# Optimization experiments

Hardware: AMD Instinct MI355X
Metric: run time of the kernel (lower is better)

The kernel has to match this reference:

```python
import jax, jax.numpy as jnp
import numpy as np

N_NODES = 500_000
N_EDGES = 16_000_000


def setup_inputs() -> dict:
    key = jax.random.key(0)
    ks = jax.random.split(key, 10)
    x = jax.random.normal(ks[0], (N_NODES, 8), dtype=jnp.float32)
    edge_index = jax.random.randint(ks[1], (2, N_EDGES), 0, N_NODES, dtype=jnp.int64)
    W1_l = jax.random.normal(ks[2], (8, 32), dtype=jnp.float32) * 0.1
    W1_r = jax.random.normal(ks[3], (8, 32), dtype=jnp.float32) * 0.1
    b1 = jax.random.normal(ks[4], (32,), dtype=jnp.float32) * 0.1
    W2_l = jax.random.normal(ks[5], (32, 16), dtype=jnp.float32) * 0.1
    W2_r = jax.random.normal(ks[6], (32, 16), dtype=jnp.float32) * 0.1
    b2 = jax.random.normal(ks[7], (16,), dtype=jnp.float32) * 0.1
    W_out = jax.random.normal(ks[8], (16, 1), dtype=jnp.float32) * 0.1
    b_out = jax.random.normal(ks[9], (1,), dtype=jnp.float32) * 0.1
    return {"x": x, "edge_index": edge_index, "W1_l": W1_l, "W1_r": W1_r, "b1": b1,
            "W2_l": W2_l, "W2_r": W2_r, "b2": b2, "W_out": W_out, "b_out": b_out}


def _sage_conv(x, src, dst, deg_inv, W_l, W_r, b):
    # mean-aggregate neighbor features: gather x[src], scatter-add to dst, divide by degree
    agg = jax.ops.segment_sum(x[src], dst, num_segments=N_NODES)  # [N, d_in]
    mean_nb = agg * deg_inv[:, None]
    return mean_nb @ W_l + x @ W_r + b


def reference(x, edge_index, W1_l, W1_r, b1, W2_l, W2_r, b2, W_out, b_out):
    src, dst = edge_index[0], edge_index[1]
    # in-degree per target node (mean aggregation denominator), clamped at 1
    deg = jax.ops.segment_sum(jnp.ones((src.shape[0],), dtype=x.dtype), dst,
                              num_segments=N_NODES)
    deg_inv = 1.0 / jnp.maximum(deg, 1.0)
    h = jax.nn.relu(_sage_conv(x, src, dst, deg_inv, W1_l, W1_r, b1))
    # dropout(p=0.1) is identity at inference
    h = jax.nn.relu(_sage_conv(h, src, dst, deg_inv, W2_l, W2_r, b2))
    return jax.nn.sigmoid(h @ W_out + b_out)  # [N, 1]
```

## Files before the change

### kernel.cpp

```cpp
#include <hip/hip_runtime.h>
#include <hip/hip_fp16.h>
#include <math.h>

#define N_NODES 500000
#define N_EDGES 16000000

#define NBUCKET 2048
#define NSB 64
#define NSLICE 32
#define NB_USED 1954
#define BUCKET_CAP 9216

#define NCH_H 500
#define CHUNK_H 32000
#define NCH_A 1000
#define CHUNK_A 16000
#define T_A 4000
#define T_B 4000

#define OFF_TOT     0
#define OFF_BASE    8192
#define OFF_FCUR    16512
#define OFF_SBCUR   24704
#define OFF_AUXB    24960
#define OFF_ROW     25600
#define OFF_HISTB   2025600
#define OFF_XH8     4025600
#define OFF_PAIRS   8025664
#define OFF_AUX     72025664
#define OFF_H1P8    72025664
#define OFF_S2      80025664
#define OFF_DEGQ    96025664

typedef float v2f __attribute__((ext_vector_type(2)));
typedef unsigned int v4u __attribute__((ext_vector_type(4)));

static __device__ inline float2 up2(unsigned int u) {
  __half2 h = *reinterpret_cast<__half2*>(&u);
  return __half22float2(h);
}
static __device__ inline unsigned int ph2(float a, float b) {
  __half2 h = __floats2half2_rn(a, b);
  return *reinterpret_cast<unsigned int*>(&h);
}
static __device__ inline unsigned int pk_fp8x4(float a, float b, float c, float d) {
  int u = __builtin_amdgcn_cvt_pk_fp8_f32(a, b, 0, false);
  u = __builtin_amdgcn_cvt_pk_fp8_f32(c, d, u, true);
  return (unsigned int)u;
}
static __device__ inline void acc8(float* a, uint2 g) {
  v2f f01 = __builtin_amdgcn_cvt_pk_f32_fp8((int)g.x, false);
  v2f f23 = __builtin_amdgcn_cvt_pk_f32_fp8((int)g.x, true);
  v2f f45 = __builtin_amdgcn_cvt_pk_f32_fp8((int)g.y, false);
  v2f f67 = __builtin_amdgcn_cvt_pk_f32_fp8((int)g.y, true);
  a[0] += f01.x; a[1] += f01.y; a[2] += f23.x; a[3] += f23.y;
  a[4] += f45.x; a[5] += f45.y; a[6] += f67.x; a[7] += f67.y;
}
static __device__ inline void acc16(float* a, uint4 g) {
  v2f f0 = __builtin_amdgcn_cvt_pk_f32_fp8((int)g.x, false);
  v2f f1 = __builtin_amdgcn_cvt_pk_f32_fp8((int)g.x, true);
  v2f f2 = __builtin_amdgcn_cvt_pk_f32_fp8((int)g.y, false);
  v2f f3 = __builtin_amdgcn_cvt_pk_f32_fp8((int)g.y, true);
  v2f f4 = __builtin_amdgcn_cvt_pk_f32_fp8((int)g.z, false);
  v2f f5 = __builtin_amdgcn_cvt_pk_f32_fp8((int)g.z, true);
  v2f f6 = __builtin_amdgcn_cvt_pk_f32_fp8((int)g.w, false);
  v2f f7 = __builtin_amdgcn_cvt_pk_f32_fp8((int)g.w, true);
  a[0] += f0.x;  a[1] += f0.y;  a[2] += f1.x;  a[3] += f1.y;
  a[4] += f2.x;  a[5] += f2.y;  a[6] += f3.x;  a[7] += f3.y;
  a[8] += f4.x;  a[9] += f4.y;  a[10] += f5.x; a[11] += f5.y;
  a[12] += f6.x; a[13] += f6.y; a[14] += f7.x; a[15] += f7.y;
}

__global__ __launch_bounds__(256) void k_xcast(const float* __restrict__ x,
                                               uint2* __restrict__ xh8) {
  int i = blockIdx.x * 256 + threadIdx.x;
  if (i >= N_NODES) return;
  const float4* xp = (const float4*)(x + (size_t)i * 8);
  float4 a = xp[0], b = xp[1];
  uint2 v;
  v.x = pk_fp8x4(a.x, a.y, a.z, a.w);
  v.y = pk_fp8x4(b.x, b.y, b.z, b.w);
  xh8[i] = v;
}

__global__ __launch_bounds__(256) void k_hist(const int* __restrict__ ei,
                                              int* __restrict__ tot) {
  __shared__ int hist[NBUCKET];
  int t = threadIdx.x;
  int c = blockIdx.x;
#pragma unroll
  for (int j = 0; j < NBUCKET / 256; j++) hist[t + j * 256] = 0;
  __syncthreads();
  int e0 = c * CHUNK_H;
  const int ng = CHUNK_H / 4;
  for (int g = t; g < ng; g += 256) {
    uint4 d4 = *(const uint4*)(ei + N_EDGES + e0 + g * 4);
    atomicAdd(&hist[d4.x >> 8], 1);
    atomicAdd(&hist[d4.y >> 8], 1);
    atomicAdd(&hist[d4.z >> 8], 1);
    atomicAdd(&hist[d4.w >> 8], 1);
  }
  __syncthreads();
#pragma unroll
  for (int j = 0; j < NBUCKET / 256; j++) {
    int b = t + j * 256;
    if (hist[b]) atomicAdd(&tot[b], hist[b]);
  }
}

__global__ __launch_bounds__(256) void k_scan(const int* __restrict__ tot,
                                              int* __restrict__ base,
                                              int* __restrict__ fineCur,
                                              int* __restrict__ sbCur,
                                              int* __restrict__ auxBase) {
  __shared__ int lds[256];
  int t = threadIdx.x;
  int loc[8];
  int s = 0;
#pragma unroll
  for (int j = 0; j < 8; j++) {
    loc[j] = s;
    s += tot[t * 8 + j];
  }
  lds[t] = s;
  __syncthreads();
  for (int off = 1; off < 256; off <<= 1) {
    int v = (t >= off) ? lds[t - off] : 0;
    __syncthreads();
    lds[t] += v;
    __syncthreads();
  }
  int eb = (t > 0) ? lds[t - 1] : 0;
#pragma unroll
  for (int j = 0; j < 8; j++) {
    int idx = t * 8 + j;
    int v = eb + loc[j];
    base[idx] = v;
    fineCur[idx] = v;
  }
  if (t == 255) base[NBUCKET] = lds[255];
  if (t < NSB) {
    int v = (t > 0) ? lds[t * 4 - 1] : 0;
    if (t >= 32) v -= lds[127];
    sbCur[t] = v;
    auxBase[t] = v;
  }
}

__global__ __launch_bounds__(256) void k_passA(const int* __restrict__ ei,
                                               int* __restrict__ sbCur,
                                               unsigned int* __restrict__ aux,
                                               int* __restrict__ histB,
                                               int half) {
  __shared__ unsigned int ldsW[T_A];
  __shared__ unsigned char sid[T_A];
  __shared__ int histA[4 * 64];
  __shared__ int hist[4 * 32];
  __shared__ int gbase[4 * 32];
  __shared__ int loff[32];
  __shared__ int lcur[32];
  __shared__ int tot_s;
  int t = threadIdx.x;
  int c = blockIdx.x;
  int e0 = c * CHUNK_A;
  int sb0 = half * 32;
  if (half == 0) {
    histA[t] = 0;
    __syncthreads();
    const int ng = CHUNK_A / 4;
    for (int g = t; g < ng; g += 256) {
      uint4 d4 = *(const uint4*)(ei + N_EDGES + e0 + g * 4);
      int tile = g / (T_A / 4);
      unsigned int dd[4] = {d4.x, d4.y, d4.z, d4.w};
#pragma unroll
      for (int j = 0; j < 4; j++)
        atomicAdd(&histA[tile * 64 + (int)(dd[j] >> 13)], 1);
    }
    __syncthreads();
    if (t < 128) {
      int ti = t >> 5, s = t & 31;
      hist[t] = histA[ti * 64 + s];
      histB[c * 128 + t] = histA[ti * 64 + 32 + s];
    }
    __syncthreads();
  } else {
    if (t < 128) hist[t] = histB[c * 128 + t];
    __syncthreads();
  }
  if (t < 32) {
    int h0 = hist[t], h1 = hist[32 + t], h2 = hist[64 + t], h3 = hist[96 + t];
    int g = atomicAdd(&sbCur[sb0 + t], h0 + h1 + h2 + h3);
    gbase[t] = g;
    gbase[32 + t] = g + h0;
    gbase[64 + t] = g + h0 + h1;
    gbase[96 + t] = g + h0 + h1 + h2;
  }
  __syncthreads();
  for (int ti = 0; ti < 4; ti++) {
    if (t == 0) {
      int r = 0;
      for (int s = 0; s < 32; s++) {
        loff[s] = r; lcur[s] = r; r += hist[ti * 32 + s];
      }
      tot_s = r;
    }
    __syncthreads();
    int tb = e0 + ti * T_A;
    const int ng = T_A / 4;
    for (int g = t; g < ng; g += 256) {
      uint4 s4 = *(const uint4*)(ei + tb + g * 4);
      uint4 d4 = *(const uint4*)(ei + N_EDGES + tb + g * 4);
      unsigned int ss[4] = {s4.x, s4.y, s4.z, s4.w};
      unsigned int dd[4] = {d4.x, d4.y, d4.z, d4.w};
#pragma unroll
      for (int j = 0; j < 4; j++) {
        int sb = (int)(dd[j] >> 13);
        if ((sb >> 5) == half) {
          int sl = sb & 31;
          int pos = atomicAdd(&lcur[sl], 1);
          ldsW[pos] = ss[j] | ((dd[j] & 8191u) << 19);
          sid[pos] = (unsigned char)sl;
        }
      }
    }
    __syncthreads();
    int tot2 = tot_s;
    for (int k = t; k < tot2; k += 256) {
      int s = sid[k];
      __builtin_nontemporal_store(ldsW[k], &aux[gbase[ti * 32 + s] + (k - loff[s])]);
    }
    __syncthreads();
  }
}

__global__ __launch_bounds__(256) void k_passB(const unsigned int* __restrict__ aux,
                                               const int* __restrict__ base,
                                               const int* __restrict__ auxBase,
                                               int* __restrict__ fineCur,
                                               unsigned int* __restrict__ pairs,
                                               int half) {
  __shared__ unsigned int ldsW[T_B];
  __shared__ unsigned char sid[T_B];
  __shared__ int hist[4 * 32];
  __shared__ int gbase[4 * 32];
  __shared__ int loff[32];
  __shared__ int lcur[32];
  __shared__ int tot_s;
  int t = threadIdx.x;
  int sbl = blockIdx.x / NSLICE;
  int sl = blockIdx.x % NSLICE;
  int sb = half * 32 + sbl;
  int aStart = auxBase[sb];
  int len = base[(sb + 1) << 5] - base[sb << 5];
  int per = (len + NSLICE - 1) / NSLICE;
  int lo = sl * per;
  int hi = lo + per;
  if (hi > len) hi = len;
  if (lo >= hi) return;
  int nt = (hi - lo + T_B - 1) / T_B;
  if (t < 128) hist[t] = 0;
  __syncthreads();
  for (int k = lo + t; k < hi; k += 256) {
    unsigned int w = aux[aStart + k];
    int tile = (k - lo) / T_B;
    atomicAdd(&hist[tile * 32 + (int)(w >> 27)], 1);
  }
  __syncthreads();
  if (t < 32) {
    int h0 = hist[t], h1 = hist[32 + t], h2 = hist[64 + t], h3 = hist[96 + t];
    int g = atomicAdd(&fineCur[(sb << 5) + t], h0 + h1 + h2 + h3);
    gbase[t] = g;
    gbase[32 + t] = g + h0;
    gbase[64 + t] = g + h0 + h1;
    gbase[96 + t] = g + h0 + h1 + h2;
  }
  __syncthreads();
  for (int ti = 0; ti < nt; ti++) {
    if (t == 0) {
      int r = 0;
      for (int s = 0; s < 32; s++) {
        loff[s] = r; lcur[s] = r; r += hist[ti * 32 + s];
      }
      tot_s = r;
    }
    __syncthreads();
    int tl = lo + ti * T_B;
    int te = tl + T_B;
    if (te > hi) te = hi;
    for (int k = tl + t; k < te; k += 256) {
      unsigned int w = aux[aStart + k];
      int s = (int)(w >> 27);
      int pos = atomicAdd(&lcur[s], 1);
      ldsW[pos] = w;
      sid[pos] = (unsigned char)s;
    }
    __syncthreads();
    int tot2 = tot_s;
    for (int k = t; k < tot2; k += 256) {
      int s = sid[k];
      __builtin_nontemporal_store(ldsW[k], &pairs[gbase[ti * 32 + s] + (k - loff[s])]);
    }
    __syncthreads();
  }
}

__global__ __launch_bounds__(256) void k_sort(unsigned int* __restrict__ pairs,
                                              const int* __restrict__ base,
                                              int* __restrict__ row,
                                              unsigned int* __restrict__ degq) {
  __shared__ unsigned int sp[BUCKET_CAP];
  __shared__ int hist[1024];
  __shared__ int cur[1024];
  __shared__ int lds[256];
  int t = threadIdx.x;
  int b = blockIdx.x;
  int e0 = base[b];
  int n = base[b + 1] - e0;
  if (n > BUCKET_CAP) n = BUCKET_CAP;
  for (int k = t; k < n; k += 256) sp[k] = pairs[e0 + k];
#pragma unroll
  for (int j = 0; j < 4; j++) hist[t + j * 256] = 0;
  __syncthreads();
  for (int k = t; k < n; k += 256) {
    unsigned int p = sp[k];
    int key = (int)(((p >> 19) & 255u) << 2) | (int)((p & 0x7FFFFu) >> 17);
    atomicAdd(&hist[key], 1);
  }
  __syncthreads();
  int h0 = hist[4 * t], h1 = hist[4 * t + 1], h2 = hist[4 * t + 2], h3 = hist[4 * t + 3];
  int s = h0 + h1 + h2 + h3;
  lds[t] = s;
  __syncthreads();
  for (int off = 1; off < 256; off <<= 1) {
    int v = (t >= off) ? lds[t - off] : 0;
    __syncthreads();
    lds[t] += v;
    __syncthreads();
  }
  int ebase = (t > 0) ? lds[t - 1] : 0;
  cur[4 * t] = e0 + ebase;
  cur[4 * t + 1] = e0 + ebase + h0;
  cur[4 * t + 2] = e0 + ebase + h0 + h1;
  cur[4 * t + 3] = e0 + ebase + h0 + h1 + h2;
  int i = (b << 8) + t;
  if (i < N_NODES) {
    row[i] = e0 + ebase;
    degq[i] = (unsigned)h0 | ((unsigned)h1 << 8) | ((unsigned)h2 << 16) |
              ((unsigned)h3 << 24);
  }
  __syncthreads();
  for (int k = t; k < n; k += 256) {
    unsigned int p = sp[k];
    int key = (int)(((p >> 19) & 255u) << 2) | (int)((p & 0x7FFFFu) >> 17);
    int pos = atomicAdd(&cur[key], 1);
    pairs[pos] = p & 0x7FFFFu;
  }
}

__global__ __launch_bounds__(256) void k_l1(
    const unsigned int* __restrict__ adj, const int* __restrict__ row,
    const unsigned int* __restrict__ degq, const uint2* __restrict__ xh8,
    const float* __restrict__ x,
    const float* __restrict__ W1l, const float* __restrict__ W1r,
    const float* __restrict__ b1,
    const float* __restrict__ W2l, const float* __restrict__ W2r,
    v4u* __restrict__ h1p8, v4u* __restrict__ s2) {
  __shared__ float sW1l[256], sW1r[256], sb1[32], sW2l[512], sW2r[512];
  int t = threadIdx.x;
  sW1l[t] = W1l[t];
  sW1r[t] = W1r[t];
  sW2l[t] = W2l[t];  sW2l[t + 256] = W2l[t + 256];
  sW2r[t] = W2r[t];  sW2r[t + 256] = W2r[t + 256];
  if (t < 32) sb1[t] = b1[t];
  __syncthreads();

  int i = blockIdx.x * 256 + t;
  if (i >= N_NODES) return;
  int rs = row[i];
  unsigned dq = degq[i];
  int d = (int)((dq & 255u) + ((dq >> 8) & 255u) + ((dq >> 16) & 255u) + (dq >> 24));

  float acc[8] = {0, 0, 0, 0, 0, 0, 0, 0};
  int j = 0;
  for (; j + 4 <= d; j += 4) {
    int a0 = (int)__builtin_nontemporal_load(&adj[rs + j + 0]);
    int a1 = (int)__builtin_nontemporal_load(&adj[rs + j + 1]);
    int a2 = (int)__builtin_nontemporal_load(&adj[rs + j + 2]);
    int a3 = (int)__builtin_nontemporal_load(&adj[rs + j + 3]);
    uint2 g0 = xh8[a0], g1 = xh8[a1], g2 = xh8[a2], g3 = xh8[a3];
    acc8(acc, g0); acc8(acc, g1); acc8(acc, g2); acc8(acc, g3);
  }
  for (; j < d; j++) {
    uint2 g = xh8[(int)__builtin_nontemporal_load(&adj[rs + j])];
    acc8(acc, g);
  }

  float dinv = 1.0f / fmaxf((float)d, 1.0f);
  float m[8];
#pragma unroll
  for (int f = 0; f < 8; f++) m[f] = acc[f] * dinv;
  const float4* xp = (const float4*)(x + (size_t)i * 8);
  float4 x0 = xp[0], x1 = xp[1];
  float xv[8] = {x0.x, x0.y, x0.z, x0.w, x1.x, x1.y, x1.z, x1.w};

  float h[32];
#pragma unroll
  for (int jj = 0; jj < 32; jj++) h[jj] = sb1[jj];
#pragma unroll
  for (int k = 0; k < 8; k++) {
#pragma unroll
    for (int jj = 0; jj < 32; jj++) {
      h[jj] = fmaf(m[k], sW1l[k * 32 + jj], h[jj]);
      h[jj] = fmaf(xv[k], sW1r[k * 32 + jj], h[jj]);
    }
  }
#pragma unroll
  for (int jj = 0; jj < 32; jj++) h[jj] = fmaxf(h[jj], 0.0f);

  float p[16], s[16];
#pragma unroll
  for (int jj = 0; jj < 16; jj++) { p[jj] = 0.0f; s[jj] = 0.0f; }
#pragma unroll
  for (int k = 0; k < 32; k++) {
#pragma unroll
    for (int jj = 0; jj < 16; jj++) {
      p[jj] = fmaf(h[k], sW2l[k * 16 + jj], p[jj]);
      s[jj] = fmaf(h[k], sW2r[k * 16 + jj], s[jj]);
    }
  }
  v4u hv;
  hv.x = pk_fp8x4(p[0], p[1], p[2], p[3]);
  hv.y = pk_fp8x4(p[4], p[5], p[6], p[7]);
  hv.z = pk_fp8x4(p[8], p[9], p[10], p[11]);
  hv.w = pk_fp8x4(p[12], p[13], p[14], p[15]);
  __builtin_nontemporal_store(hv, &h1p8[i]);
  v4u slo, shi;
  slo.x = ph2(s[0], s[1]);   slo.y = ph2(s[2], s[3]);
  slo.z = ph2(s[4], s[5]);   slo.w = ph2(s[6], s[7]);
  shi.x = ph2(s[8], s[9]);   shi.y = ph2(s[10], s[11]);
  shi.z = ph2(s[12], s[13]); shi.w = ph2(s[14], s[15]);
  __builtin_nontemporal_store(slo, &s2[(size_t)i * 2]);
  __builtin_nontemporal_store(shi, &s2[(size_t)i * 2 + 1]);
}

__global__ __launch_bounds__(256) void k_l2(
    const unsigned int* __restrict__ adj, const int* __restrict__ row,
    const unsigned int* __restrict__ degq, const uint4* __restrict__ h1p8,
    const v4u* __restrict__ s2, const float* __restrict__ b2,
    const float* __restrict__ Wout, const float* __restrict__ bout,
    float* __restrict__ out) {
  __shared__ float sb2[16], sWo[16], sbo;
  int t = threadIdx.x;
  if (t < 16) { sb2[t] = b2[t]; sWo[t] = Wout[t]; }
  if (t == 0) sbo = bout[0];
  __syncthreads();

  int i = blockIdx.x * 256 + t;
  bool act = i < N_NODES;
  int rs = act ? row[i] : 0;
  unsigned dq = act ? degq[i] : 0;
  int d = (int)((dq & 255u) + ((dq >> 8) & 255u) + ((dq >> 16) & 255u) + (dq >> 24));

  float acc[16];
#pragma unroll
  for (int jj = 0; jj < 16; jj++) acc[jj] = 0.0f;
  int off = 0;
#pragma unroll
  for (int q = 0; q < 4; q++) {
    int len = (int)((dq >> (8 * q)) & 255u);
    int js = rs + off;
    int j = 0;
    for (; j + 4 <= len; j += 4) {
      int a0 = (int)__builtin_nontemporal_load(&adj[js + j + 0]);
      int a1 = (int)__builtin_nontemporal_load(&adj[js + j + 1]);
      int a2 = (int)__builtin_nontemporal_load(&adj[js + j + 2]);
      int a3 = (int)__builtin_nontemporal_load(&adj[js + j + 3]);
      uint4 g0 = h1p8[a0], g1 = h1p8[a1], g2 = h1p8[a2], g3 = h1p8[a3];
      acc16(acc, g0); acc16(acc, g1); acc16(acc, g2); acc16(acc, g3);
    }
    for (; j < len; j++) {
      uint4 g = h1p8[(int)__builtin_nontemporal_load(&adj[js + j])];
      acc16(acc, g);
    }
    off += len;
    if (q < 3) __syncthreads();
  }

  if (!act) return;
  float dinv = 1.0f / fmaxf((float)d, 1.0f);
  v4u q0 = __builtin_nontemporal_load(&s2[(size_t)i * 2]);
  v4u q1 = __builtin_nontemporal_load(&s2[(size_t)i * 2 + 1]);
  float2 s0 = up2(q0.x), s1 = up2(q0.y), s2v = up2(q0.z), s3 = up2(q0.w);
  float2 s4 = up2(q1.x), s5 = up2(q1.y), s6 = up2(q1.z), s7 = up2(q1.w);
  float sv[16] = {s0.x, s0.y, s1.x, s1.y, s2v.x, s2v.y, s3.x, s3.y,
                  s4.x, s4.y, s5.x, s5.y, s6.x, s6.y, s7.x, s7.y};
  float o = sbo;
#pragma unroll
  for (int c = 0; c < 16; c++) {
    float h2 = fmaxf(acc[c] * dinv + sv[c] + sb2[c], 0.0f);
    o = fmaf(h2, sWo[c], o);
  }
  out[i] = 1.0f / (1.0f + expf(-o));
}

extern "C" void kernel_launch(void* const* d_in, const int* in_sizes, int n_in,
                              void* d_out, int out_size, void* d_ws, size_t ws_size,
                              hipStream_t stream) {
  const float* x    = (const float*)d_in[0];
  const int*   ei   = (const int*)d_in[1];
  const float* W1l  = (const float*)d_in[2];
  const float* W1r  = (const float*)d_in[3];
  const float* b1   = (const float*)d_in[4];
  const float* W2l  = (const float*)d_in[5];
  const float* W2r  = (const float*)d_in[6];
  const float* b2   = (const float*)d_in[7];
  const float* Wout = (const float*)d_in[8];
  const float* bout = (const float*)d_in[9];
  float* out = (float*)d_out;

  char* ws = (char*)d_ws;
  int* tot     = (int*)(ws + OFF_TOT);
  int* base    = (int*)(ws + OFF_BASE);
  int* fineCur = (int*)(ws + OFF_FCUR);
  int* sbCur   = (int*)(ws + OFF_SBCUR);
  int* auxBase = (int*)(ws + OFF_AUXB);
  int* row     = (int*)(ws + OFF_ROW);
  int* histB   = (int*)(ws + OFF_HISTB);
  uint2* xh8   = (uint2*)(ws + OFF_XH8);
  unsigned int* pairs = (unsigned int*)(ws + OFF_PAIRS);
  unsigned int* aux   = (unsigned int*)(ws + OFF_AUX);
  v4u* h1p8    = (v4u*)(ws + OFF_H1P8);
  v4u* s2      = (v4u*)(ws + OFF_S2);
  unsigned int* degq = (unsigned int*)(ws + OFF_DEGQ);

  (void)hipMemsetAsync(tot, 0, NBUCKET * sizeof(int), stream);

  k_xcast<<<NB_USED, 256, 0, stream>>>(x, xh8);
  k_hist<<<NCH_H, 256, 0, stream>>>(ei, tot);
  k_scan<<<1, 256, 0, stream>>>(tot, base, fineCur, sbCur, auxBase);
  k_passA<<<NCH_A, 256, 0, stream>>>(ei, sbCur, aux, histB, 0);
  k_passB<<<32 * NSLICE, 256, 0, stream>>>(aux, base, auxBase, fineCur, pairs, 0);
  k_passA<<<NCH_A, 256, 0, stream>>>(ei, sbCur, aux, histB, 1);
  k_passB<<<32 * NSLICE, 256, 0, stream>>>(aux, base, auxBase, fineCur, pairs, 1);
  k_sort<<<NBUCKET, 256, 0, stream>>>(pairs, base, row, degq);
  k_l1<<<NB_USED, 256, 0, stream>>>(pairs, row, degq, xh8, x, W1l, W1r, b1,
                                    W2l, W2r, h1p8, s2);
  k_l2<<<NB_USED, 256, 0, stream>>>(pairs, row, degq, (const uint4*)h1p8, s2,
                                    b2, Wout, bout, out);
}
```

Before: 828.6 us.

## Fuse fine-bucket scatter into per-bucket sort and merge histogram passes

The global destination histogram and the per-tile superbucket histogram are now computed in one counting kernel, so passA no longer re-reads destinations in its first half. The separate passB scatter and k_sort kernels are replaced by k_passC. In k_passC, each block scans its whole superbucket slice of aux and uses wave ballot compaction to collect only the entries belonging to its fine bucket into LDS, then sorts them locally. This removes a global write and re-read of the pairs array and a kernel launch. In exchange, each superbucket is read redundantly by 32 blocks, which relies on cache reuse to stay cheap.

Measured after the change: 2.643 ms. 219% more time.

```diff
diff --git a/kernel.cpp b/kernel.cpp
--- a/kernel.cpp
+++ b/kernel.cpp
@@ -7,30 +7,25 @@
 
 #define NBUCKET 2048
 #define NSB 64
-#define NSLICE 32
 #define NB_USED 1954
 #define BUCKET_CAP 9216
 
-#define NCH_H 500
-#define CHUNK_H 32000
 #define NCH_A 1000
 #define CHUNK_A 16000
 #define T_A 4000
-#define T_B 4000
 
 #define OFF_TOT     0
 #define OFF_BASE    8192
-#define OFF_FCUR    16512
 #define OFF_SBCUR   24704
 #define OFF_AUXB    24960
 #define OFF_ROW     25600
-#define OFF_HISTB   2025600
+#define OFF_DEGQ    2025600
 #define OFF_XH8     4025600
 #define OFF_PAIRS   8025664
+#define OFF_HISTB   71001664
 #define OFF_AUX     72025664
 #define OFF_H1P8    72025664
 #define OFF_S2      80025664
-#define OFF_DEGQ    96025664
 
 typedef float v2f __attribute__((ext_vector_type(2)));
 typedef unsigned int v4u __attribute__((ext_vector_type(4)));
@@ -83,34 +78,43 @@
   xh8[i] = v;
 }
 
-__global__ __launch_bounds__(256) void k_hist(const int* __restrict__ ei,
-                                              int* __restrict__ tot) {
-  __shared__ int hist[NBUCKET];
+__global__ __launch_bounds__(256) void k_count(const int* __restrict__ ei,
+                                               int* __restrict__ tot,
+                                               int* __restrict__ histB) {
+  __shared__ int fh[NBUCKET];
+  __shared__ int sbh[4 * 64];
   int t = threadIdx.x;
   int c = blockIdx.x;
 #pragma unroll
-  for (int j = 0; j < NBUCKET / 256; j++) hist[t + j * 256] = 0;
-  __syncthreads();
-  int e0 = c * CHUNK_H;
-  const int ng = CHUNK_H / 4;
+  for (int j = 0; j < NBUCKET / 256; j++) fh[t + j * 256] = 0;
+  sbh[t] = 0;
+  __syncthreads();
+  int e0 = c * CHUNK_A;
+  const int ng = CHUNK_A / 4;
   for (int g = t; g < ng; g += 256) {
     uint4 d4 = *(const uint4*)(ei + N_EDGES + e0 + g * 4);
-    atomicAdd(&hist[d4.x >> 8], 1);
-    atomicAdd(&hist[d4.y >> 8], 1);
-    atomicAdd(&hist[d4.z >> 8], 1);
-    atomicAdd(&hist[d4.w >> 8], 1);
+    int tile = g / (T_A / 4);
+    unsigned int dd[4] = {d4.x, d4.y, d4.z, d4.w};
+#pragma unroll
+    for (int j = 0; j < 4; j++) {
+      atomicAdd(&fh[dd[j] >> 8], 1);
+      atomicAdd(&sbh[tile * 64 + (int)(dd[j] >> 13)], 1);
+    }
   }
   __syncthreads();
 #pragma unroll
   for (int j = 0; j < NBUCKET / 256; j++) {
     int b = t + j * 256;
-    if (hist[b]) atomicAdd(&tot[b], hist[b]);
+    if (fh[b]) atomicAdd(&tot[b], fh[b]);
+  }
+  {
+    int ti = t >> 6, sb64 = t & 63;
+    histB[c * 256 + (sb64 >> 5) * 128 + ti * 32 + (sb64 & 31)] = sbh[ti * 64 + sb64];
   }
 }
 
 __global__ __launch_bounds__(256) void k_scan(const int* __restrict__ tot,
                                               int* __restrict__ base,
-                                              int* __restrict__ fineCur,
                                               int* __restrict__ sbCur,
                                               int* __restrict__ auxBase) {
   __shared__ int lds[256];
@@ -132,12 +136,7 @@
   }
   int eb = (t > 0) ? lds[t - 1] : 0;
 #pragma unroll
-  for (int j = 0; j < 8; j++) {
-    int idx = t * 8 + j;
-    int v = eb + loc[j];
-    base[idx] = v;
-    fineCur[idx] = v;
-  }
+  for (int j = 0; j < 8; j++) base[t * 8 + j] = eb + loc[j];
   if (t == 255) base[NBUCKET] = lds[255];
   if (t < NSB) {
     int v = (t > 0) ? lds[t * 4 - 1] : 0;
@@ -150,11 +149,10 @@
 __global__ __launch_bounds__(256) void k_passA(const int* __restrict__ ei,
                                                int* __restrict__ sbCur,
                                                unsigned int* __restrict__ aux,
-                                               int* __restrict__ histB,
+                                               const int* __restrict__ histB,
                                                int half) {
   __shared__ unsigned int ldsW[T_A];
   __shared__ unsigned char sid[T_A];
-  __shared__ int histA[4 * 64];
   __shared__ int hist[4 * 32];
   __shared__ int gbase[4 * 32];
   __shared__ int loff[32];
@@ -164,29 +162,8 @@
   int c = blockIdx.x;
   int e0 = c * CHUNK_A;
   int sb0 = half * 32;
-  if (half == 0) {
-    histA[t] = 0;
-    __syncthreads();
-    const int ng = CHUNK_A / 4;
-    for (int g = t; g < ng; g += 256) {
-      uint4 d4 = *(const uint4*)(ei + N_EDGES + e0 + g * 4);
-      int tile = g / (T_A / 4);
-      unsigned int dd[4] = {d4.x, d4.y, d4.z, d4.w};
-#pragma unroll
-      for (int j = 0; j < 4; j++)
-        atomicAdd(&histA[tile * 64 + (int)(dd[j] >> 13)], 1);
-    }
-    __syncthreads();
-    if (t < 128) {
-      int ti = t >> 5, s = t & 31;
-      hist[t] = histA[ti * 64 + s];
-      histB[c * 128 + t] = histA[ti * 64 + 32 + s];
-    }
-    __syncthreads();
-  } else {
-    if (t < 128) hist[t] = histB[c * 128 + t];
-    __syncthreads();
-  }
+  if (t < 128) hist[t] = histB[c * 256 + half * 128 + t];
+  __syncthreads();
   if (t < 32) {
     int h0 = hist[t], h1 = hist[32 + t], h2 = hist[64 + t], h3 = hist[96 + t];
     int g = atomicAdd(&sbCur[sb0 + t], h0 + h1 + h2 + h3);
@@ -233,94 +210,55 @@
   }
 }
 
-__global__ __launch_bounds__(256) void k_passB(const unsigned int* __restrict__ aux,
+__global__ __launch_bounds__(256) void k_passC(const unsigned int* __restrict__ aux,
                                                const int* __restrict__ base,
                                                const int* __restrict__ auxBase,
-                                               int* __restrict__ fineCur,
                                                unsigned int* __restrict__ pairs,
+                                               int* __restrict__ row,
+                                               unsigned int* __restrict__ degq,
                                                int half) {
-  __shared__ unsigned int ldsW[T_B];
-  __shared__ unsigned char sid[T_B];
-  __shared__ int hist[4 * 32];
-  __shared__ int gbase[4 * 32];
-  __shared__ int loff[32];
-  __shared__ int lcur[32];
-  __shared__ int tot_s;
-  int t = threadIdx.x;
-  int sbl = blockIdx.x / NSLICE;
-  int sl = blockIdx.x % NSLICE;
-  int sb = half * 32 + sbl;
-  int aStart = auxBase[sb];
-  int len = base[(sb + 1) << 5] - base[sb << 5];
-  int per = (len + NSLICE - 1) / NSLICE;
-  int lo = sl * per;
-  int hi = lo + per;
-  if (hi > len) hi = len;
-  if (lo >= hi) return;
-  int nt = (hi - lo + T_B - 1) / T_B;
-  if (t < 128) hist[t] = 0;
-  __syncthreads();
-  for (int k = lo + t; k < hi; k += 256) {
-    unsigned int w = aux[aStart + k];
-    int tile = (k - lo) / T_B;
-    atomicAdd(&hist[tile * 32 + (int)(w >> 27)], 1);
-  }
-  __syncthreads();
-  if (t < 32) {
-    int h0 = hist[t], h1 = hist[32 + t], h2 = hist[64 + t], h3 = hist[96 + t];
-    int g = atomicAdd(&fineCur[(sb << 5) + t], h0 + h1 + h2 + h3);
-    gbase[t] = g;
-    gbase[32 + t] = g + h0;
-    gbase[64 + t] = g + h0 + h1;
-    gbase[96 + t] = g + h0 + h1 + h2;
-  }
-  __syncthreads();
-  for (int ti = 0; ti < nt; ti++) {
-    if (t == 0) {
-      int r = 0;
-      for (int s = 0; s < 32; s++) {
-        loff[s] = r; lcur[s] = r; r += hist[ti * 32 + s];
-      }
-      tot_s = r;
-    }
-    __syncthreads();
-    int tl = lo + ti * T_B;
-    int te = tl + T_B;
-    if (te > hi) te = hi;
-    for (int k = tl + t; k < te; k += 256) {
-      unsigned int w = aux[aStart + k];
-      int s = (int)(w >> 27);
-      int pos = atomicAdd(&lcur[s], 1);
-      ldsW[pos] = w;
-      sid[pos] = (unsigned char)s;
-    }
-    __syncthreads();
-    int tot2 = tot_s;
-    for (int k = t; k < tot2; k += 256) {
-      int s = sid[k];
-      __builtin_nontemporal_store(ldsW[k], &pairs[gbase[ti * 32 + s] + (k - loff[s])]);
-    }
-    __syncthreads();
-  }
-}
-
-__global__ __launch_bounds__(256) void k_sort(unsigned int* __restrict__ pairs,
-                                              const int* __restrict__ base,
-                                              int* __restrict__ row,
-                                              unsigned int* __restrict__ degq) {
   __shared__ unsigned int sp[BUCKET_CAP];
   __shared__ int hist[1024];
   __shared__ int cur[1024];
   __shared__ int lds[256];
-  int t = threadIdx.x;
-  int b = blockIdx.x;
-  int e0 = base[b];
-  int n = base[b + 1] - e0;
+  __shared__ int cnt;
+  int t = threadIdx.x;
+  int idx = blockIdx.x;
+  int sbl = (idx & 7) | (((idx >> 8) & 3) << 3);
+  int fl = (idx >> 3) & 31;
+  int sb = half * 32 + sbl;
+  int aStart = auxBase[sb];
+  int len = base[(sb + 1) << 5] - base[sb << 5];
+  int fb = (sb << 5) + fl;
+  int e0 = base[fb];
+  if (t == 0) cnt = 0;
+#pragma unroll
+  for (int j = 0; j < 4; j++) hist[t + j * 256] = 0;
+  __syncthreads();
+  int lane = t & 63;
+  unsigned long long ltm = (1ull << lane) - 1ull;
+  int nit = (len + 255) >> 8;
+  for (int it = 0; it < nit; it++) {
+    int k = (it << 8) + t;
+    unsigned int w = 0;
+    bool mine = false;
+    if (k < len) {
+      w = aux[aStart + k];
+      mine = ((w >> 19) >> 8) == (unsigned)fl;
+    }
+    unsigned long long m = __ballot(mine);
+    if (mine) {
+      int leader = __ffsll(m) - 1;
+      int bs = 0;
+      if (lane == leader) bs = atomicAdd(&cnt, (int)__popcll(m));
+      bs = __shfl(bs, leader);
+      int pos = bs + (int)__popcll(m & ltm);
+      if (pos < BUCKET_CAP) sp[pos] = w;
+    }
+  }
+  __syncthreads();
+  int n = cnt;
   if (n > BUCKET_CAP) n = BUCKET_CAP;
-  for (int k = t; k < n; k += 256) sp[k] = pairs[e0 + k];
-#pragma unroll
-  for (int j = 0; j < 4; j++) hist[t + j * 256] = 0;
-  __syncthreads();
   for (int k = t; k < n; k += 256) {
     unsigned int p = sp[k];
     int key = (int)(((p >> 19) & 255u) << 2) | (int)((p & 0x7FFFFu) >> 17);
@@ -342,7 +280,7 @@
   cur[4 * t + 1] = e0 + ebase + h0;
   cur[4 * t + 2] = e0 + ebase + h0 + h1;
   cur[4 * t + 3] = e0 + ebase + h0 + h1 + h2;
-  int i = (b << 8) + t;
+  int i = (fb << 8) + t;
   if (i < N_NODES) {
     row[i] = e0 + ebase;
     degq[i] = (unsigned)h0 | ((unsigned)h1 << 8) | ((unsigned)h2 << 16) |
@@ -521,28 +459,26 @@
   char* ws = (char*)d_ws;
   int* tot     = (int*)(ws + OFF_TOT);
   int* base    = (int*)(ws + OFF_BASE);
-  int* fineCur = (int*)(ws + OFF_FCUR);
   int* sbCur   = (int*)(ws + OFF_SBCUR);
   int* auxBase = (int*)(ws + OFF_AUXB);
   int* row     = (int*)(ws + OFF_ROW);
+  unsigned int* degq = (unsigned int*)(ws + OFF_DEGQ);
   int* histB   = (int*)(ws + OFF_HISTB);
   uint2* xh8   = (uint2*)(ws + OFF_XH8);
   unsigned int* pairs = (unsigned int*)(ws + OFF_PAIRS);
   unsigned int* aux   = (unsigned int*)(ws + OFF_AUX);
   v4u* h1p8    = (v4u*)(ws + OFF_H1P8);
   v4u* s2      = (v4u*)(ws + OFF_S2);
-  unsigned int* degq = (unsigned int*)(ws + OFF_DEGQ);
 
   (void)hipMemsetAsync(tot, 0, NBUCKET * sizeof(int), stream);
 
   k_xcast<<<NB_USED, 256, 0, stream>>>(x, xh8);
-  k_hist<<<NCH_H, 256, 0, stream>>>(ei, tot);
-  k_scan<<<1, 256, 0, stream>>>(tot, base, fineCur, sbCur, auxBase);
+  k_count<<<NCH_A, 256, 0, stream>>>(ei, tot, histB);
+  k_scan<<<1, 256, 0, stream>>>(tot, base, sbCur, auxBase);
   k_passA<<<NCH_A, 256, 0, stream>>>(ei, sbCur, aux, histB, 0);
-  k_passB<<<32 * NSLICE, 256, 0, stream>>>(aux, base, auxBase, fineCur, pairs, 0);
+  k_passC<<<1024, 256, 0, stream>>>(aux, base, auxBase, pairs, row, degq, 0);
   k_passA<<<NCH_A, 256, 0, stream>>>(ei, sbCur, aux, histB, 1);
-  k_passB<<<32 * NSLICE, 256, 0, stream>>>(aux, base, auxBase, fineCur, pairs, 1);
-  k_sort<<<NBUCKET, 256, 0, stream>>>(pairs, base, row, degq);
+  k_passC<<<1024, 256, 0, stream>>>(aux, base, auxBase, pairs, row, degq, 1);
   k_l1<<<NB_USED, 256, 0, stream>>>(pairs, row, degq, xh8, x, W1l, W1r, b1,
                                     W2l, W2r, h1p8, s2);
   k_l2<<<NB_USED, 256, 0, stream>>>(pairs, row, degq, (const uint4*)h1p8, s2,
```
